# Kernel optimization log

Measured on AMD Instinct MI355X. Metric: run time of the kernel, lower is better.

Reference implementation:

```python
import jax, jax.numpy as jnp
import numpy as np

B, S, D, H, O, E, K = 4, 2048, 1024, 2048, 1024, 8, 2

def setup_inputs() -> dict:
    key = jax.random.key(0)
    ks = jax.random.split(key, 8)
    x = jax.random.normal(ks[0], (B, S, D), dtype=jnp.float32)
    # kaiming-uniform-ish scale for weights, zero biases (as in _init_w)
    gate_w = jax.random.uniform(ks[1], (E, D), dtype=jnp.float32, minval=-1, maxval=1) * np.sqrt(6.0 / D)
    gate_b = jnp.zeros((E,), dtype=jnp.float32)
    w1 = jax.random.uniform(ks[2], (E, D, H), dtype=jnp.float32, minval=-1, maxval=1) * np.sqrt(6.0 / D)
    b1 = jnp.zeros((E, H), dtype=jnp.float32)
    w2 = jax.random.uniform(ks[3], (E, H, O), dtype=jnp.float32, minval=-1, maxval=1) * np.sqrt(6.0 / H)
    b2 = jnp.zeros((E, O), dtype=jnp.float32)
    return {"x": x, "gate_w": gate_w, "gate_b": gate_b, "w1": w1, "b1": b1, "w2": w2, "b2": b2}

def reference(x, gate_w, gate_b, w1, b1, w2, b2):
    # gate: softmax over experts, then top-k (k=2)
    logits = jnp.einsum('bsd,ed->bse', x, gate_w) + gate_b          # [B,S,E]
    probs = jax.nn.softmax(logits, axis=-1)
    topk_vals, topk_idx = jax.lax.top_k(probs, K)                    # [B,S,K]
    # dense all-expert MLPs (Linear-ReLU-Linear), dropout = 0
    h = jax.nn.relu(jnp.einsum('bsd,edh->bseh', x, w1) + b1)         # [B,S,E,H]
    expert_out = jnp.einsum('bseh,eho->bseo', h, w2) + b2            # [B,S,E,O]
    # gather top-k experts and combine with gate weights
    sel = jnp.take_along_axis(expert_out, topk_idx[..., None], axis=2)  # [B,S,K,O]
    return jnp.sum(sel * topk_vals[..., None], axis=2)               # [B,S,O]
```

## Files before the change

kernel.cpp:

```cpp
#include <hip/hip_runtime.h>

#define T_TOKENS 8192
#define D_DIM 1024
#define H_DIM 2048
#define O_DIM 1024
#define E_NUM 8
#define NPAIR 16384

typedef unsigned short u16;
typedef __bf16 bf16x8 __attribute__((ext_vector_type(8)));
typedef float f32x4 __attribute__((ext_vector_type(4)));

__device__ inline u16 f2bf(float f) {
  union { float f; unsigned u; } v; v.f = f;
  unsigned r = v.u + 0x7FFFu + ((v.u >> 16) & 1u);
  return (u16)(r >> 16);
}

__device__ __forceinline__ void gload16(const u16* g, u16* l) {
  __builtin_amdgcn_global_load_lds((const __attribute__((address_space(1))) void*)g,
                                   (__attribute__((address_space(3))) void*)l, 16, 0, 0);
}

__global__ void transpose_cvt_kernel(const float* __restrict__ w, u16* __restrict__ wt,
                                     int R, int C) {
  __shared__ float tile[32][33];
  int e = blockIdx.z;
  int c0 = blockIdx.x * 32, r0 = blockIdx.y * 32;
  const float* wp = w + (size_t)e * R * C;
  u16* wtp = wt + (size_t)e * R * C;
  int tx = threadIdx.x, ty = threadIdx.y;
  #pragma unroll
  for (int j = 0; j < 32; j += 8)
    tile[ty + j][tx] = wp[(size_t)(r0 + ty + j) * C + c0 + tx];
  __syncthreads();
  #pragma unroll
  for (int j = 0; j < 32; j += 8)
    wtp[(size_t)(c0 + ty + j) * R + r0 + tx] = f2bf(tile[tx][ty + j]);
}

__global__ void gate_kernel(const float* __restrict__ x, const float* __restrict__ gw,
                            const float* __restrict__ gb, int* __restrict__ topk_idx,
                            float* __restrict__ topk_val, u16* __restrict__ xb) {
  int t = blockIdx.x * 4 + (threadIdx.x >> 6);
  int lane = threadIdx.x & 63;
  const float4* xr4 = (const float4*)(x + (size_t)t * D_DIM);
  const float4* gw4 = (const float4*)gw;
  u16* xbr = xb + (size_t)t * D_DIM;
  float acc[E_NUM];
  #pragma unroll
  for (int e = 0; e < E_NUM; e++) acc[e] = 0.f;
  #pragma unroll
  for (int it = 0; it < D_DIM / 256; ++it) {
    float4 xv = xr4[it * 64 + lane];
    ushort4 o;
    o.x = f2bf(xv.x); o.y = f2bf(xv.y); o.z = f2bf(xv.z); o.w = f2bf(xv.w);
    *(ushort4*)(xbr + (it * 64 + lane) * 4) = o;
    #pragma unroll
    for (int e = 0; e < E_NUM; e++) {
      float4 wv = gw4[e * (D_DIM / 4) + it * 64 + lane];
      acc[e] += xv.x * wv.x + xv.y * wv.y + xv.z * wv.z + xv.w * wv.w;
    }
  }
  #pragma unroll
  for (int e = 0; e < E_NUM; e++) {
    #pragma unroll
    for (int o = 32; o > 0; o >>= 1) acc[e] += __shfl_down(acc[e], o);
  }
  if (lane == 0) {
    float l[E_NUM], mx = -1e30f;
    #pragma unroll
    for (int e = 0; e < E_NUM; e++) { l[e] = acc[e] + gb[e]; mx = fmaxf(mx, l[e]); }
    float p[E_NUM], s = 0.f;
    #pragma unroll
    for (int e = 0; e < E_NUM; e++) { p[e] = expf(l[e] - mx); s += p[e]; }
    float inv = 1.f / s;
    int i1 = 0;
    #pragma unroll
    for (int e = 1; e < E_NUM; e++) if (p[e] > p[i1]) i1 = e;
    int i2 = (i1 == 0) ? 1 : 0;
    #pragma unroll
    for (int e = 0; e < E_NUM; e++) if (e != i1 && e != i2 && p[e] > p[i2]) i2 = e;
    topk_idx[t * 2] = i1;     topk_idx[t * 2 + 1] = i2;
    topk_val[t * 2] = p[i1] * inv; topk_val[t * 2 + 1] = p[i2] * inv;
  }
}

__global__ void histscan_kernel(const int* __restrict__ topk_idx,
                                int* __restrict__ counts, int* __restrict__ eoff) {
  __shared__ int wh[4][E_NUM];
  int tid = threadIdx.x;
  int lane = tid & 63, wave = tid >> 6;
  int myc = 0;
  for (int i = tid; i < NPAIR; i += 256) {
    int e = topk_idx[i];
    #pragma unroll
    for (int ee = 0; ee < E_NUM; ee++) {
      unsigned long long m = __ballot(e == ee);
      if (lane == ee) myc += __popcll(m);
    }
  }
  if (lane < E_NUM) wh[wave][lane] = myc;
  __syncthreads();
  if (tid == 0) {
    int s = 0;
    for (int e = 0; e < E_NUM; e++) {
      int c = wh[0][e] + wh[1][e] + wh[2][e] + wh[3][e];
      counts[e] = c;
      eoff[e] = s;
      s += c;
    }
    eoff[E_NUM] = s;
  }
}

__global__ void scatter_kernel(const int* __restrict__ topk_idx, const float* __restrict__ topk_val,
                               const int* __restrict__ eoff, int* __restrict__ cursor_pad,
                               int* __restrict__ pair_token, float* __restrict__ pair_gate) {
  __shared__ int lhist[E_NUM];
  __shared__ int lbase[E_NUM];
  int tid = threadIdx.x;
  int t = blockIdx.x * 256 + tid;
  if (tid < E_NUM) lhist[tid] = 0;
  __syncthreads();
  int e0 = topk_idx[t * 2], e1 = topk_idx[t * 2 + 1];
  int r0 = atomicAdd(&lhist[e0], 1);
  int r1 = atomicAdd(&lhist[e1], 1);
  __syncthreads();
  if (tid < E_NUM) lbase[tid] = eoff[tid] + atomicAdd(&cursor_pad[tid * 32], lhist[tid]);
  __syncthreads();
  int p0 = lbase[e0] + r0;
  int p1 = lbase[e1] + r1;
  pair_token[p0] = t; pair_gate[p0] = topk_val[t * 2];
  pair_token[p1] = t; pair_gate[p1] = topk_val[t * 2 + 1];
}


__global__ __launch_bounds__(256, 3) void gemm1_kernel(
    const u16* __restrict__ xb, const u16* __restrict__ w1t, const float* __restrict__ b1,
    const int* __restrict__ pair_token, const int* __restrict__ eoff,
    const int* __restrict__ ecnt, u16* __restrict__ hbuf) {
  const int e = blockIdx.z;
  const int ne = ecnt[e];
  const int m0t = blockIdx.y * 128;
  if (m0t >= ne) return;
  const int off = eoff[e];
  const int n0 = blockIdx.x * 128;

  __shared__ __align__(16) u16 As[128 * 64];
  __shared__ __align__(16) u16 Bs[128 * 64];

  const int tid = threadIdx.x;
  const int wid = tid >> 6;
  const int lane = tid & 63;

  const int strow8 = lane >> 3;
  const int slot = lane & 7;
  const u16* aptr[4]; const u16* bptr[4];
  u16* lA[4]; u16* lB[4];
  #pragma unroll
  for (int j = 0; j < 4; j++) {
    int r = wid * 32 + j * 8 + strow8;
    int gm = m0t + r;
    int tok = (gm < ne) ? pair_token[off + gm] : 0;
    int gl = slot ^ (r & 7);
    aptr[j] = xb + (size_t)tok * D_DIM + gl * 8;
    bptr[j] = w1t + ((size_t)e * H_DIM + (n0 + r)) * D_DIM + gl * 8;
    lA[j] = As + wid * 2048 + j * 512;
    lB[j] = Bs + wid * 2048 + j * 512;
  }

  const int wm = (wid & 1) * 64;
  const int wn = (wid >> 1) * 64;
  const int lrow = lane & 15;
  const int quad = lane >> 4;
  const int pg0 = quad ^ (lrow & 7);
  const int pg1 = (quad + 4) ^ (lrow & 7);

  f32x4 acc[4][4] = {};

  for (int k0 = 0; k0 < D_DIM; k0 += 64) {
    #pragma unroll
    for (int j = 0; j < 4; j++) { gload16(aptr[j] + k0, lA[j]); gload16(bptr[j] + k0, lB[j]); }
    __syncthreads();
    {
      bf16x8 af[4], bfr[4];
      #pragma unroll
      for (int i = 0; i < 4; i++) af[i] = *(const bf16x8*)&As[(wm + i * 16 + lrow) * 64 + pg0 * 8];
      #pragma unroll
      for (int j = 0; j < 4; j++) bfr[j] = *(const bf16x8*)&Bs[(wn + j * 16 + lrow) * 64 + pg0 * 8];
      #pragma unroll
      for (int i = 0; i < 4; i++)
        #pragma unroll
        for (int j = 0; j < 4; j++)
          acc[i][j] = __builtin_amdgcn_mfma_f32_16x16x32_bf16(af[i], bfr[j], acc[i][j], 0, 0, 0);
    }
    {
      bf16x8 af[4], bfr[4];
      #pragma unroll
      for (int i = 0; i < 4; i++) af[i] = *(const bf16x8*)&As[(wm + i * 16 + lrow) * 64 + pg1 * 8];
      #pragma unroll
      for (int j = 0; j < 4; j++) bfr[j] = *(const bf16x8*)&Bs[(wn + j * 16 + lrow) * 64 + pg1 * 8];
      #pragma unroll
      for (int i = 0; i < 4; i++)
        #pragma unroll
        for (int j = 0; j < 4; j++)
          acc[i][j] = __builtin_amdgcn_mfma_f32_16x16x32_bf16(af[i], bfr[j], acc[i][j], 0, 0, 0);
    }
    __syncthreads();
  }
  #pragma unroll
  for (int i = 0; i < 4; i++) {
    #pragma unroll
    for (int r = 0; r < 4; r++) {
      int m = wm + i * 16 + quad * 4 + r;
      int gm = m0t + m;
      if (gm >= ne) continue;
      size_t rowbase = (size_t)(off + gm) * H_DIM;
      #pragma unroll
      for (int j = 0; j < 4; j++) {
        int n = n0 + wn + j * 16 + lrow;
        float v = acc[i][j][r] + b1[e * H_DIM + n];
        v = v > 0.f ? v : 0.f;
        hbuf[rowbase + n] = f2bf(v);
      }
    }
  }
}

__global__ __launch_bounds__(256, 3) void gemm2_kernel(
    const u16* __restrict__ hbuf, const u16* __restrict__ w2t, const float* __restrict__ b2,
    const int* __restrict__ pair_token, const float* __restrict__ pair_gate,
    const int* __restrict__ eoff, const int* __restrict__ ecnt, float* __restrict__ out) {
  const int e = blockIdx.z;
  const int ne = ecnt[e];
  const int m0t = blockIdx.y * 128;
  if (m0t >= ne) return;
  const int off = eoff[e];
  const int n0 = blockIdx.x * 128;

  __shared__ __align__(16) u16 As[128 * 64];
  __shared__ __align__(16) u16 Bs[128 * 64];

  const int tid = threadIdx.x;
  const int wid = tid >> 6;
  const int lane = tid & 63;

  const int strow8 = lane >> 3;
  const int slot = lane & 7;
  const u16* aptr[4]; const u16* bptr[4];
  u16* lA[4]; u16* lB[4];
  #pragma unroll
  for (int j = 0; j < 4; j++) {
    int r = wid * 32 + j * 8 + strow8;
    int gl = slot ^ (r & 7);
    aptr[j] = hbuf + (size_t)(off + m0t + r) * H_DIM + gl * 8;
    bptr[j] = w2t + ((size_t)e * O_DIM + (n0 + r)) * H_DIM + gl * 8;
    lA[j] = As + wid * 2048 + j * 512;
    lB[j] = Bs + wid * 2048 + j * 512;
  }

  const int wm = (wid & 1) * 64;
  const int wn = (wid >> 1) * 64;
  const int lrow = lane & 15;
  const int quad = lane >> 4;
  const int pg0 = quad ^ (lrow & 7);
  const int pg1 = (quad + 4) ^ (lrow & 7);

  f32x4 acc[4][4] = {};

  for (int k0 = 0; k0 < H_DIM; k0 += 64) {
    #pragma unroll
    for (int j = 0; j < 4; j++) { gload16(aptr[j] + k0, lA[j]); gload16(bptr[j] + k0, lB[j]); }
    __syncthreads();
    {
      bf16x8 af[4], bfr[4];
      #pragma unroll
      for (int i = 0; i < 4; i++) af[i] = *(const bf16x8*)&As[(wm + i * 16 + lrow) * 64 + pg0 * 8];
      #pragma unroll
      for (int j = 0; j < 4; j++) bfr[j] = *(const bf16x8*)&Bs[(wn + j * 16 + lrow) * 64 + pg0 * 8];
      #pragma unroll
      for (int i = 0; i < 4; i++)
        #pragma unroll
        for (int j = 0; j < 4; j++)
          acc[i][j] = __builtin_amdgcn_mfma_f32_16x16x32_bf16(af[i], bfr[j], acc[i][j], 0, 0, 0);
    }
    {
      bf16x8 af[4], bfr[4];
      #pragma unroll
      for (int i = 0; i < 4; i++) af[i] = *(const bf16x8*)&As[(wm + i * 16 + lrow) * 64 + pg1 * 8];
      #pragma unroll
      for (int j = 0; j < 4; j++) bfr[j] = *(const bf16x8*)&Bs[(wn + j * 16 + lrow) * 64 + pg1 * 8];
      #pragma unroll
      for (int i = 0; i < 4; i++)
        #pragma unroll
        for (int j = 0; j < 4; j++)
          acc[i][j] = __builtin_amdgcn_mfma_f32_16x16x32_bf16(af[i], bfr[j], acc[i][j], 0, 0, 0);
    }
    __syncthreads();
  }
  #pragma unroll
  for (int i = 0; i < 4; i++) {
    #pragma unroll
    for (int r = 0; r < 4; r++) {
      int m = wm + i * 16 + quad * 4 + r;
      int gm = m0t + m;
      if (gm >= ne) continue;
      int pair = off + gm;
      int tok = pair_token[pair];
      float g = pair_gate[pair];
      #pragma unroll
      for (int j = 0; j < 4; j++) {
        int n = n0 + wn + j * 16 + lrow;
        float v = (acc[i][j][r] + b2[e * O_DIM + n]) * g;
        atomicAdd(&out[(size_t)tok * O_DIM + n], v);
      }
    }
  }
}

extern "C" void kernel_launch(void* const* d_in, const int* in_sizes, int n_in,
                              void* d_out, int out_size, void* d_ws, size_t ws_size,
                              hipStream_t stream) {
  const float* x  = (const float*)d_in[0];
  const float* gw = (const float*)d_in[1];
  const float* gb = (const float*)d_in[2];
  const float* w1 = (const float*)d_in[3];
  const float* b1 = (const float*)d_in[4];
  const float* w2 = (const float*)d_in[5];
  const float* b2 = (const float*)d_in[6];
  float* out = (float*)d_out;

  char* ws = (char*)d_ws;
  size_t off = 0;
  auto take = [&](size_t bytes) -> char* {
    char* p = ws + off;
    off = (off + bytes + 255) & ~(size_t)255;
    return p;
  };
  int*   meta       = (int*)take(2048);
  int*   cursor_pad = meta;
  int*   counts     = meta + 256;
  int*   eoff       = meta + 264;
  int*   topk_idx   = (int*)take((size_t)T_TOKENS * 2 * 4);
  float* topk_val   = (float*)take((size_t)T_TOKENS * 2 * 4);
  int*   pair_token = (int*)take((size_t)(NPAIR + 256) * 4);
  float* pair_gate  = (float*)take((size_t)(NPAIR + 256) * 4);
  u16*   xb         = (u16*)take((size_t)T_TOKENS * D_DIM * 2);
  u16*   w1t        = (u16*)take((size_t)E_NUM * D_DIM * H_DIM * 2);
  u16*   w2t        = (u16*)take((size_t)E_NUM * H_DIM * O_DIM * 2);
  u16*   hbuf       = (u16*)take((size_t)(NPAIR + 128) * H_DIM * 2);

  hipMemsetAsync(meta, 0, 2048, stream);
  hipMemsetAsync(out, 0, (size_t)T_TOKENS * O_DIM * 4, stream);

  transpose_cvt_kernel<<<dim3(H_DIM / 32, D_DIM / 32, E_NUM), dim3(32, 8), 0, stream>>>(w1, w1t, D_DIM, H_DIM);
  transpose_cvt_kernel<<<dim3(O_DIM / 32, H_DIM / 32, E_NUM), dim3(32, 8), 0, stream>>>(w2, w2t, H_DIM, O_DIM);
  gate_kernel<<<T_TOKENS / 4, 256, 0, stream>>>(x, gw, gb, topk_idx, topk_val, xb);
  histscan_kernel<<<1, 256, 0, stream>>>(topk_idx, counts, eoff);
  scatter_kernel<<<T_TOKENS / 256, 256, 0, stream>>>(topk_idx, topk_val, eoff, cursor_pad, pair_token, pair_gate);
  gemm1_kernel<<<dim3(H_DIM / 128, NPAIR / 128, E_NUM), 256, 0, stream>>>(xb, w1t, b1, pair_token, eoff, counts, hbuf);
  gemm2_kernel<<<dim3(O_DIM / 128, NPAIR / 128, E_NUM), 256, 0, stream>>>(hbuf, w2t, b2, pair_token, pair_gate, eoff, counts, out);
}
```

Baseline: 490.0 us.

## Compact MoE GEMM grid via tile table, double-buffer LDS, swizzle block order

The histogram kernel now builds a compact table of (expert, row-tile) pairs. Both grouped GEMMs launch a fixed 136-row grid indexed through this table instead of an E×NPAIR/128 grid that is mostly empty blocks that exit early. The GEMM main loops double-buffer the LDS tiles so the global→LDS loads for the next K slice overlap the MFMA work on the current one. Block indices are swizzled so consecutive blocks spread across the N tiles. This doubles LDS use and lowers launch_bounds occupancy from 3 to 2 blocks per CU.

```diff
diff --git a/kernel.cpp b/kernel.cpp
--- a/kernel.cpp
+++ b/kernel.cpp
@@ -6,6 +6,7 @@
 #define O_DIM 1024
 #define E_NUM 8
 #define NPAIR 16384
+#define GY_MAX 136
 
 typedef unsigned short u16;
 typedef __bf16 bf16x8 __attribute__((ext_vector_type(8)));
@@ -87,7 +88,9 @@
 }
 
 __global__ void histscan_kernel(const int* __restrict__ topk_idx,
-                                int* __restrict__ counts, int* __restrict__ eoff) {
+                                int* __restrict__ counts, int* __restrict__ eoff,
+                                int* __restrict__ nblk, int* __restrict__ tbl_e,
+                                int* __restrict__ tbl_m0) {
   __shared__ int wh[4][E_NUM];
   int tid = threadIdx.x;
   int lane = tid & 63, wave = tid >> 6;
@@ -103,14 +106,19 @@
   if (lane < E_NUM) wh[wave][lane] = myc;
   __syncthreads();
   if (tid == 0) {
-    int s = 0;
+    int s = 0, cl[E_NUM];
     for (int e = 0; e < E_NUM; e++) {
       int c = wh[0][e] + wh[1][e] + wh[2][e] + wh[3][e];
       counts[e] = c;
+      cl[e] = c;
       eoff[e] = s;
       s += c;
     }
     eoff[E_NUM] = s;
+    int nb = 0;
+    for (int e = 0; e < E_NUM; e++)
+      for (int m0 = 0; m0 < cl[e]; m0 += 128) { tbl_e[nb] = e; tbl_m0[nb] = m0; nb++; }
+    nblk[0] = nb;
   }
 }
 
@@ -136,19 +144,25 @@
 }
 
 
-__global__ __launch_bounds__(256, 3) void gemm1_kernel(
+__global__ __launch_bounds__(256, 2) void gemm1_kernel(
     const u16* __restrict__ xb, const u16* __restrict__ w1t, const float* __restrict__ b1,
     const int* __restrict__ pair_token, const int* __restrict__ eoff,
-    const int* __restrict__ ecnt, u16* __restrict__ hbuf) {
-  const int e = blockIdx.z;
+    const int* __restrict__ ecnt, const int* __restrict__ nblk,
+    const int* __restrict__ tbl_e, const int* __restrict__ tbl_m0,
+    u16* __restrict__ hbuf) {
+  int lin = blockIdx.y * 16 + blockIdx.x;
+  int swz = (lin & 7) * (16 * GY_MAX / 8) + (lin >> 3);
+  const int bx = swz & 15;
+  const int yb = swz >> 4;
+  if (yb >= nblk[0]) return;
+  const int e = tbl_e[yb];
+  const int m0t = tbl_m0[yb];
   const int ne = ecnt[e];
-  const int m0t = blockIdx.y * 128;
-  if (m0t >= ne) return;
   const int off = eoff[e];
-  const int n0 = blockIdx.x * 128;
-
-  __shared__ __align__(16) u16 As[128 * 64];
-  __shared__ __align__(16) u16 Bs[128 * 64];
+  const int n0 = bx * 128;
+
+  __shared__ __align__(16) u16 As0[128 * 64], As1[128 * 64];
+  __shared__ __align__(16) u16 Bs0[128 * 64], Bs1[128 * 64];
 
   const int tid = threadIdx.x;
   const int wid = tid >> 6;
@@ -157,7 +171,6 @@
   const int strow8 = lane >> 3;
   const int slot = lane & 7;
   const u16* aptr[4]; const u16* bptr[4];
-  u16* lA[4]; u16* lB[4];
   #pragma unroll
   for (int j = 0; j < 4; j++) {
     int r = wid * 32 + j * 8 + strow8;
@@ -166,8 +179,6 @@
     int gl = slot ^ (r & 7);
     aptr[j] = xb + (size_t)tok * D_DIM + gl * 8;
     bptr[j] = w1t + ((size_t)e * H_DIM + (n0 + r)) * D_DIM + gl * 8;
-    lA[j] = As + wid * 2048 + j * 512;
-    lB[j] = Bs + wid * 2048 + j * 512;
   }
 
   const int wm = (wid & 1) * 64;
@@ -179,36 +190,46 @@
 
   f32x4 acc[4][4] = {};
 
-  for (int k0 = 0; k0 < D_DIM; k0 += 64) {
-    #pragma unroll
-    for (int j = 0; j < 4; j++) { gload16(aptr[j] + k0, lA[j]); gload16(bptr[j] + k0, lB[j]); }
+  auto STAGE = [&](u16* A_, u16* B_, int kk) {
+    #pragma unroll
+    for (int j = 0; j < 4; j++) {
+      gload16(aptr[j] + kk, A_ + wid * 2048 + j * 512);
+      gload16(bptr[j] + kk, B_ + wid * 2048 + j * 512);
+    }
+  };
+  auto COMPUTE = [&](const u16* A_, const u16* B_) {
+    bf16x8 af[4], bfr[4];
+    #pragma unroll
+    for (int i = 0; i < 4; i++) af[i] = *(const bf16x8*)&A_[(wm + i * 16 + lrow) * 64 + pg0 * 8];
+    #pragma unroll
+    for (int j = 0; j < 4; j++) bfr[j] = *(const bf16x8*)&B_[(wn + j * 16 + lrow) * 64 + pg0 * 8];
+    #pragma unroll
+    for (int i = 0; i < 4; i++)
+      #pragma unroll
+      for (int j = 0; j < 4; j++)
+        acc[i][j] = __builtin_amdgcn_mfma_f32_16x16x32_bf16(af[i], bfr[j], acc[i][j], 0, 0, 0);
+    #pragma unroll
+    for (int i = 0; i < 4; i++) af[i] = *(const bf16x8*)&A_[(wm + i * 16 + lrow) * 64 + pg1 * 8];
+    #pragma unroll
+    for (int j = 0; j < 4; j++) bfr[j] = *(const bf16x8*)&B_[(wn + j * 16 + lrow) * 64 + pg1 * 8];
+    #pragma unroll
+    for (int i = 0; i < 4; i++)
+      #pragma unroll
+      for (int j = 0; j < 4; j++)
+        acc[i][j] = __builtin_amdgcn_mfma_f32_16x16x32_bf16(af[i], bfr[j], acc[i][j], 0, 0, 0);
+  };
+
+  STAGE(As0, Bs0, 0);
+  __syncthreads();
+  for (int k0 = 0; k0 < D_DIM; k0 += 128) {
+    if (k0 + 64 < D_DIM) STAGE(As1, Bs1, k0 + 64);
+    COMPUTE(As0, Bs0);
     __syncthreads();
-    {
-      bf16x8 af[4], bfr[4];
-      #pragma unroll
-      for (int i = 0; i < 4; i++) af[i] = *(const bf16x8*)&As[(wm + i * 16 + lrow) * 64 + pg0 * 8];
-      #pragma unroll
-      for (int j = 0; j < 4; j++) bfr[j] = *(const bf16x8*)&Bs[(wn + j * 16 + lrow) * 64 + pg0 * 8];
-      #pragma unroll
-      for (int i = 0; i < 4; i++)
-        #pragma unroll
-        for (int j = 0; j < 4; j++)
-          acc[i][j] = __builtin_amdgcn_mfma_f32_16x16x32_bf16(af[i], bfr[j], acc[i][j], 0, 0, 0);
-    }
-    {
-      bf16x8 af[4], bfr[4];
-      #pragma unroll
-      for (int i = 0; i < 4; i++) af[i] = *(const bf16x8*)&As[(wm + i * 16 + lrow) * 64 + pg1 * 8];
-      #pragma unroll
-      for (int j = 0; j < 4; j++) bfr[j] = *(const bf16x8*)&Bs[(wn + j * 16 + lrow) * 64 + pg1 * 8];
-      #pragma unroll
-      for (int i = 0; i < 4; i++)
-        #pragma unroll
-        for (int j = 0; j < 4; j++)
-          acc[i][j] = __builtin_amdgcn_mfma_f32_16x16x32_bf16(af[i], bfr[j], acc[i][j], 0, 0, 0);
-    }
+    if (k0 + 128 < D_DIM) STAGE(As0, Bs0, k0 + 128);
+    COMPUTE(As1, Bs1);
     __syncthreads();
   }
+
   #pragma unroll
   for (int i = 0; i < 4; i++) {
     #pragma unroll
@@ -228,19 +249,25 @@
   }
 }
 
-__global__ __launch_bounds__(256, 3) void gemm2_kernel(
+__global__ __launch_bounds__(256, 2) void gemm2_kernel(
     const u16* __restrict__ hbuf, const u16* __restrict__ w2t, const float* __restrict__ b2,
     const int* __restrict__ pair_token, const float* __restrict__ pair_gate,
-    const int* __restrict__ eoff, const int* __restrict__ ecnt, float* __restrict__ out) {
-  const int e = blockIdx.z;
+    const int* __restrict__ eoff, const int* __restrict__ ecnt,
+    const int* __restrict__ nblk, const int* __restrict__ tbl_e,
+    const int* __restrict__ tbl_m0, float* __restrict__ out) {
+  int lin = blockIdx.y * 8 + blockIdx.x;
+  int swz = (lin & 7) * (8 * GY_MAX / 8) + (lin >> 3);
+  const int bx = swz & 7;
+  const int yb = swz >> 3;
+  if (yb >= nblk[0]) return;
+  const int e = tbl_e[yb];
+  const int m0t = tbl_m0[yb];
   const int ne = ecnt[e];
-  const int m0t = blockIdx.y * 128;
-  if (m0t >= ne) return;
   const int off = eoff[e];
-  const int n0 = blockIdx.x * 128;
-
-  __shared__ __align__(16) u16 As[128 * 64];
-  __shared__ __align__(16) u16 Bs[128 * 64];
+  const int n0 = bx * 128;
+
+  __shared__ __align__(16) u16 As0[128 * 64], As1[128 * 64];
+  __shared__ __align__(16) u16 Bs0[128 * 64], Bs1[128 * 64];
 
   const int tid = threadIdx.x;
   const int wid = tid >> 6;
@@ -249,15 +276,12 @@
   const int strow8 = lane >> 3;
   const int slot = lane & 7;
   const u16* aptr[4]; const u16* bptr[4];
-  u16* lA[4]; u16* lB[4];
   #pragma unroll
   for (int j = 0; j < 4; j++) {
     int r = wid * 32 + j * 8 + strow8;
     int gl = slot ^ (r & 7);
     aptr[j] = hbuf + (size_t)(off + m0t + r) * H_DIM + gl * 8;
     bptr[j] = w2t + ((size_t)e * O_DIM + (n0 + r)) * H_DIM + gl * 8;
-    lA[j] = As + wid * 2048 + j * 512;
-    lB[j] = Bs + wid * 2048 + j * 512;
   }
 
   const int wm = (wid & 1) * 64;
@@ -269,36 +293,46 @@
 
   f32x4 acc[4][4] = {};
 
-  for (int k0 = 0; k0 < H_DIM; k0 += 64) {
-    #pragma unroll
-    for (int j = 0; j < 4; j++) { gload16(aptr[j] + k0, lA[j]); gload16(bptr[j] + k0, lB[j]); }
+  auto STAGE = [&](u16* A_, u16* B_, int kk) {
+    #pragma unroll
+    for (int j = 0; j < 4; j++) {
+      gload16(aptr[j] + kk, A_ + wid * 2048 + j * 512);
+      gload16(bptr[j] + kk, B_ + wid * 2048 + j * 512);
+    }
+  };
+  auto COMPUTE = [&](const u16* A_, const u16* B_) {
+    bf16x8 af[4], bfr[4];
+    #pragma unroll
+    for (int i = 0; i < 4; i++) af[i] = *(const bf16x8*)&A_[(wm + i * 16 + lrow) * 64 + pg0 * 8];
+    #pragma unroll
+    for (int j = 0; j < 4; j++) bfr[j] = *(const bf16x8*)&B_[(wn + j * 16 + lrow) * 64 + pg0 * 8];
+    #pragma unroll
+    for (int i = 0; i < 4; i++)
+      #pragma unroll
+      for (int j = 0; j < 4; j++)
+        acc[i][j] = __builtin_amdgcn_mfma_f32_16x16x32_bf16(af[i], bfr[j], acc[i][j], 0, 0, 0);
+    #pragma unroll
+    for (int i = 0; i < 4; i++) af[i] = *(const bf16x8*)&A_[(wm + i * 16 + lrow) * 64 + pg1 * 8];
+    #pragma unroll
+    for (int j = 0; j < 4; j++) bfr[j] = *(const bf16x8*)&B_[(wn + j * 16 + lrow) * 64 + pg1 * 8];
+    #pragma unroll
+    for (int i = 0; i < 4; i++)
+      #pragma unroll
+      for (int j = 0; j < 4; j++)
+        acc[i][j] = __builtin_amdgcn_mfma_f32_16x16x32_bf16(af[i], bfr[j], acc[i][j], 0, 0, 0);
+  };
+
+  STAGE(As0, Bs0, 0);
+  __syncthreads();
+  for (int k0 = 0; k0 < H_DIM; k0 += 128) {
+    if (k0 + 64 < H_DIM) STAGE(As1, Bs1, k0 + 64);
+    COMPUTE(As0, Bs0);
     __syncthreads();
-    {
-      bf16x8 af[4], bfr[4];
-      #pragma unroll
-      for (int i = 0; i < 4; i++) af[i] = *(const bf16x8*)&As[(wm + i * 16 + lrow) * 64 + pg0 * 8];
-      #pragma unroll
-      for (int j = 0; j < 4; j++) bfr[j] = *(const bf16x8*)&Bs[(wn + j * 16 + lrow) * 64 + pg0 * 8];
-      #pragma unroll
-      for (int i = 0; i < 4; i++)
-        #pragma unroll
-        for (int j = 0; j < 4; j++)
-          acc[i][j] = __builtin_amdgcn_mfma_f32_16x16x32_bf16(af[i], bfr[j], acc[i][j], 0, 0, 0);
-    }
-    {
-      bf16x8 af[4], bfr[4];
-      #pragma unroll
-      for (int i = 0; i < 4; i++) af[i] = *(const bf16x8*)&As[(wm + i * 16 + lrow) * 64 + pg1 * 8];
-      #pragma unroll
-      for (int j = 0; j < 4; j++) bfr[j] = *(const bf16x8*)&Bs[(wn + j * 16 + lrow) * 64 + pg1 * 8];
-      #pragma unroll
-      for (int i = 0; i < 4; i++)
-        #pragma unroll
-        for (int j = 0; j < 4; j++)
-          acc[i][j] = __builtin_amdgcn_mfma_f32_16x16x32_bf16(af[i], bfr[j], acc[i][j], 0, 0, 0);
-    }
+    if (k0 + 128 < H_DIM) STAGE(As0, Bs0, k0 + 128);
+    COMPUTE(As1, Bs1);
     __syncthreads();
   }
+
   #pragma unroll
   for (int i = 0; i < 4; i++) {
     #pragma unroll
@@ -338,10 +372,13 @@
     off = (off + bytes + 255) & ~(size_t)255;
     return p;
   };
-  int*   meta       = (int*)take(2048);
+  int*   meta       = (int*)take(4096);
   int*   cursor_pad = meta;
   int*   counts     = meta + 256;
   int*   eoff       = meta + 264;
+  int*   nblk       = meta + 273;
+  int*   tbl_e      = meta + 274;
+  int*   tbl_m0     = meta + 410;
   int*   topk_idx   = (int*)take((size_t)T_TOKENS * 2 * 4);
   float* topk_val   = (float*)take((size_t)T_TOKENS * 2 * 4);
   int*   pair_token = (int*)take((size_t)(NPAIR + 256) * 4);
@@ -351,14 +388,14 @@
   u16*   w2t        = (u16*)take((size_t)E_NUM * H_DIM * O_DIM * 2);
   u16*   hbuf       = (u16*)take((size_t)(NPAIR + 128) * H_DIM * 2);
 
-  hipMemsetAsync(meta, 0, 2048, stream);
+  hipMemsetAsync(meta, 0, 4096, stream);
   hipMemsetAsync(out, 0, (size_t)T_TOKENS * O_DIM * 4, stream);
 
   transpose_cvt_kernel<<<dim3(H_DIM / 32, D_DIM / 32, E_NUM), dim3(32, 8), 0, stream>>>(w1, w1t, D_DIM, H_DIM);
   transpose_cvt_kernel<<<dim3(O_DIM / 32, H_DIM / 32, E_NUM), dim3(32, 8), 0, stream>>>(w2, w2t, H_DIM, O_DIM);
   gate_kernel<<<T_TOKENS / 4, 256, 0, stream>>>(x, gw, gb, topk_idx, topk_val, xb);
-  histscan_kernel<<<1, 256, 0, stream>>>(topk_idx, counts, eoff);
+  histscan_kernel<<<1, 256, 0, stream>>>(topk_idx, counts, eoff, nblk, tbl_e, tbl_m0);
   scatter_kernel<<<T_TOKENS / 256, 256, 0, stream>>>(topk_idx, topk_val, eoff, cursor_pad, pair_token, pair_gate);
-  gemm1_kernel<<<dim3(H_DIM / 128, NPAIR / 128, E_NUM), 256, 0, stream>>>(xb, w1t, b1, pair_token, eoff, counts, hbuf);
-  gemm2_kernel<<<dim3(O_DIM / 128, NPAIR / 128, E_NUM), 256, 0, stream>>>(hbuf, w2t, b2, pair_token, pair_gate, eoff, counts, out);
-}
+  gemm1_kernel<<<dim3(16, GY_MAX), 256, 0, stream>>>(xb, w1t, b1, pair_token, eoff, counts, nblk, tbl_e, tbl_m0, hbuf);
+  gemm2_kernel<<<dim3(8, GY_MAX), 256, 0, stream>>>(hbuf, w2t, b2, pair_token, pair_gate, eoff, counts, nblk, tbl_e, tbl_m0, out);
+}
```

Measured after the change: 523.7 us. 6.9% more time.
